# Kernel tuning notes

Hardware: AMD Instinct MI355X
Metric: run time of the kernel (lower is better)

## Reference

```python
import jax, jax.numpy as jnp
import numpy as np

D_MAX = 6.4
MASS = 40.0
GRAV = 9.8
N_PARTS = 4
B, NPTS, H, W = 512, 2048, 256, 256


def _interp(grid, xy):
    # grid: (B,H,W) over [-D_MAX,D_MAX]^2; xy: (B,N,2) -> (B,N,1) bilinear
    Bg, Hg, Wg = grid.shape
    gi = jnp.clip((xy[..., 0] + D_MAX) / (2.0 * D_MAX) * (Hg - 1), 0.0, Hg - 1.0)
    gj = jnp.clip((xy[..., 1] + D_MAX) / (2.0 * D_MAX) * (Wg - 1), 0.0, Wg - 1.0)
    i0 = jnp.clip(jnp.floor(gi).astype(jnp.int32), 0, Hg - 2)
    j0 = jnp.clip(jnp.floor(gj).astype(jnp.int32), 0, Wg - 2)
    wi = gi - i0.astype(grid.dtype)
    wj = gj - j0.astype(grid.dtype)
    flat = grid.reshape(Bg, Hg * Wg)
    gat = lambda ii, jj: jnp.take_along_axis(flat, ii * Wg + jj, axis=1)
    v = (gat(i0, j0) * (1 - wi) * (1 - wj) + gat(i0, j0 + 1) * (1 - wi) * wj
         + gat(i0 + 1, j0) * wi * (1 - wj) + gat(i0 + 1, j0 + 1) * wi * wj)
    return v[..., None]


def setup_inputs() -> dict:
    key = jax.random.key(0)
    ks = jax.random.split(key, 12)
    x = jax.random.uniform(ks[0], (B, 3), jnp.float32, -2.0, 2.0)
    xd = jax.random.normal(ks[1], (B, 3), jnp.float32)
    R, _ = jnp.linalg.qr(jax.random.normal(ks[2], (B, 3, 3), jnp.float32))
    omega = jax.random.normal(ks[3], (B, 3), jnp.float32) * 0.5
    A = jax.random.normal(ks[4], (B, 3, 3), jnp.float32) * 0.3
    I = jnp.einsum('bij,bkj->bik', A, A) + 2.0 * jnp.eye(3, dtype=jnp.float32)
    robot_points = jax.random.normal(ks[5], (B, NPTS, 3), jnp.float32) * 0.3
    z_grid = jax.random.normal(ks[6], (B, H, W), jnp.float32) * 0.1
    z_grid_grad = jax.random.normal(ks[7], (B, 2, H, W), jnp.float32) * 0.2
    stiffness = jax.random.uniform(ks[8], (B, H, W), jnp.float32, 500.0, 2000.0)
    damping = jax.random.uniform(ks[9], (B, H, W), jnp.float32, 10.0, 100.0)
    friction = jax.random.uniform(ks[10], (B, H, W), jnp.float32, 0.2, 1.0)
    driving_parts = jax.random.randint(ks[11], (NPTS,), 0, N_PARTS, jnp.int32)
    controls = jax.random.normal(jax.random.fold_in(key, 99), (B, N_PARTS), jnp.float32) * 2.0
    return dict(x=x, xd=xd, R=R, omega=omega, I=I, robot_points=robot_points,
                z_grid=z_grid, z_grid_grad=z_grid_grad, stiffness=stiffness,
                damping=damping, friction=friction, driving_parts=driving_parts,
                controls=controls)


def reference(x, xd, R, omega, I, robot_points, z_grid, z_grid_grad,
              stiffness, damping, friction, driving_parts, controls):
    n_pts = robot_points.shape[1]
    # local_to_global
    x_points = jnp.einsum('bij,bnj->bni', R, robot_points) + x[:, None]  # (B,N,3)
    xy = x_points[..., :2]
    z_points = _interp(z_grid, xy)              # (B,N,1)
    k_pts = _interp(stiffness, xy)
    d_pts = _interp(damping, xy)
    mu_pts = _interp(friction, xy)
    dh = x_points[..., 2:3] - z_points
    on_grid = ((x_points[..., 0:1] >= -D_MAX) & (x_points[..., 0:1] <= D_MAX)
               & (x_points[..., 1:2] >= -D_MAX) & (x_points[..., 1:2] <= D_MAX))
    in_contact = ((dh <= 0.0) & on_grid).astype(x.dtype)
    # surface normals from heightmap gradient: n = normalize([-dz/dx, -dz/dy, 1])
    gx = _interp(z_grid_grad[:, 0], xy)
    gy = _interp(z_grid_grad[:, 1], xy)
    n = jnp.concatenate([-gx, -gy, jnp.ones_like(gx)], axis=-1)
    n = n / jnp.linalg.norm(n, axis=-1, keepdims=True)
    # point velocities
    xd_points = xd[:, None] + jnp.cross(omega[:, None], x_points - x[:, None])
    xd_points_n = jnp.sum(xd_points * n, axis=-1, keepdims=True)
    F_spring = -(k_pts * dh + d_pts * xd_points_n) * n
    F_spring = F_spring * in_contact / n_pts
    thrust_dir = R[..., 0] / jnp.linalg.norm(R[..., 0], axis=-1, keepdims=True)
    Nmag = jnp.linalg.norm(F_spring, axis=2)  # (B,N)
    F_friction = jnp.zeros_like(F_spring)
    for i in range(N_PARTS):
        v_cmd = controls[:, i:i + 1] * thrust_dir          # (B,3)
        dv = v_cmd[:, None] - xd_points                     # (B,N,3)
        dv_n = jnp.sum(dv * n, axis=-1, keepdims=True)
        dv_tau = dv - dv_n * n
        Fi = mu_pts * Nmag[..., None] * jnp.tanh(dv_tau)
        mask = (driving_parts == i)[None, :, None]
        F_friction = jnp.where(mask, Fi, F_friction)
    torque = jnp.sum(jnp.cross(x_points - x[:, None], F_spring + F_friction), axis=1)
    I_inv = jnp.linalg.inv(I)
    omega_d = jnp.einsum('bij,bj->bi', I_inv, torque)
    F_grav = jnp.array([0.0, 0.0, -MASS * GRAV], dtype=x.dtype)
    F_cog = F_grav + F_spring.sum(axis=1) + F_friction.sum(axis=1)
    xdd = F_cog / MASS
    return (xd, xdd, omega_d, F_spring, F_friction)
```

## Files before the change

### kernel.cpp

```cpp
#include <hip/hip_runtime.h>

#pragma clang fp contract(off)

static constexpr int Bc    = 512;
static constexpr int NPTSc = 2048;
static constexpr int Hc    = 256;
static constexpr int Wc    = 256;
static constexpr float DMAXF = 6.4f;
static constexpr int CELLS = 2048;

__device__ __forceinline__ float bl(float g00, float g01, float g10, float g11,
                                    float wi, float wj) {
#pragma clang fp contract(off)
    return g00 * (1.0f - wi) * (1.0f - wj)
         + g01 * (1.0f - wi) * wj
         + g10 * wi * (1.0f - wj)
         + g11 * wi * wj;
}

__global__ __launch_bounds__(256)
void phys_points(const float* __restrict__ x, const float* __restrict__ xd,
                 const float* __restrict__ R, const float* __restrict__ omega,
                 const float* __restrict__ rp,
                 const float* __restrict__ zg, const float* __restrict__ zgg,
                 const float* __restrict__ kg, const float* __restrict__ dg,
                 const float* __restrict__ mug,
                 const int* __restrict__ dparts, const float* __restrict__ ctrl,
                 float* __restrict__ outFs, float* __restrict__ outFf,
                 float* __restrict__ partial)
{
#pragma clang fp contract(off)
    __shared__ float sg[6 * CELLS];
    __shared__ int sbox[4];

    const int tid = threadIdx.x;
    const int b = blockIdx.x >> 3;
    const int n = ((blockIdx.x & 7) << 8) + tid;

    float xb0 = x[b * 3 + 0], xb1 = x[b * 3 + 1], xb2 = x[b * 3 + 2];
    float xd0 = xd[b * 3 + 0], xd1 = xd[b * 3 + 1], xd2 = xd[b * 3 + 2];
    float om0 = omega[b * 3 + 0], om1 = omega[b * 3 + 1], om2 = omega[b * 3 + 2];
    float R00 = R[b * 9 + 0], R01 = R[b * 9 + 1], R02 = R[b * 9 + 2];
    float R10 = R[b * 9 + 3], R11 = R[b * 9 + 4], R12 = R[b * 9 + 5];
    float R20 = R[b * 9 + 6], R21 = R[b * 9 + 7], R22 = R[b * 9 + 8];

    const int part = dparts[n];
    const float cpart = ctrl[b * 4 + part];

    const int pbase = (b * NPTSc + n) * 3;
    float p0 = rp[pbase + 0], p1 = rp[pbase + 1], p2 = rp[pbase + 2];

    float xp0 = (R00 * p0 + R01 * p1 + R02 * p2) + xb0;
    float xp1 = (R10 * p0 + R11 * p1 + R12 * p2) + xb1;
    float xp2 = (R20 * p0 + R21 * p1 + R22 * p2) + xb2;

    float rx = xp0 - xb0, ry = xp1 - xb1, rz = xp2 - xb2;

    float gi = (xp0 + DMAXF) / (2.0f * DMAXF) * 255.0f;
    gi = fminf(fmaxf(gi, 0.0f), 255.0f);
    float gj = (xp1 + DMAXF) / (2.0f * DMAXF) * 255.0f;
    gj = fminf(fmaxf(gj, 0.0f), 255.0f);
    int i0 = (int)floorf(gi); i0 = min(max(i0, 0), Hc - 2);
    int j0 = (int)floorf(gj); j0 = min(max(j0, 0), Wc - 2);
    float wi = gi - (float)i0;
    float wj = gj - (float)j0;

    int mni = i0, mxi = i0, mnj = j0, mxj = j0;
    #pragma unroll
    for (int off = 32; off > 0; off >>= 1) {
        mni = min(mni, __shfl_xor(mni, off, 64));
        mxi = max(mxi, __shfl_xor(mxi, off, 64));
        mnj = min(mnj, __shfl_xor(mnj, off, 64));
        mxj = max(mxj, __shfl_xor(mxj, off, 64));
    }
    if (tid == 0) { sbox[0] = 255; sbox[1] = 0; sbox[2] = 255; sbox[3] = 0; }
    __syncthreads();
    if ((tid & 63) == 0) {
        atomicMin(&sbox[0], mni); atomicMax(&sbox[1], mxi);
        atomicMin(&sbox[2], mnj); atomicMax(&sbox[3], mxj);
    }
    __syncthreads();
    const int bmin_i = sbox[0], bmin_j = sbox[2];
    const int ih = sbox[1] - bmin_i + 2;
    const int jw = sbox[3] - bmin_j + 2;
    const bool use_lds = (ih * jw) <= CELLS;

    const int gb  = b * (Hc * Wc);
    const int gb2 = b * (2 * Hc * Wc);
    const float* planes[6] = { zg + gb, kg + gb, dg + gb, mug + gb,
                               zgg + gb2, zgg + gb2 + Hc * Wc };

    float cv[6][4];
    if (use_lds) {
        const int tx = tid & 63, ty = tid >> 6;
        #pragma unroll
        for (int p = 0; p < 6; ++p) {
            const float* src = planes[p] + bmin_i * Wc + bmin_j;
            float* dst = sg + p * CELLS;
            for (int r = ty; r < ih; r += 4)
                for (int c = tx; c < jw; c += 64)
                    dst[r * jw + c] = src[r * Wc + c];
        }
        __syncthreads();
        const int la = (i0 - bmin_i) * jw + (j0 - bmin_j);
        #pragma unroll
        for (int p = 0; p < 6; ++p) {
            const float* s = sg + p * CELLS + la;
            cv[p][0] = s[0]; cv[p][1] = s[1];
            cv[p][2] = s[jw]; cv[p][3] = s[jw + 1];
        }
    } else {
        const int la = i0 * Wc + j0;
        #pragma unroll
        for (int p = 0; p < 6; ++p) {
            const float* s = planes[p] + la;
            cv[p][0] = s[0]; cv[p][1] = s[1];
            cv[p][2] = s[Wc]; cv[p][3] = s[Wc + 1];
        }
    }

    float zp  = bl(cv[0][0], cv[0][1], cv[0][2], cv[0][3], wi, wj);
    float kp  = bl(cv[1][0], cv[1][1], cv[1][2], cv[1][3], wi, wj);
    float dpv = bl(cv[2][0], cv[2][1], cv[2][2], cv[2][3], wi, wj);
    float mup = bl(cv[3][0], cv[3][1], cv[3][2], cv[3][3], wi, wj);
    float gx  = bl(cv[4][0], cv[4][1], cv[4][2], cv[4][3], wi, wj);
    float gy  = bl(cv[5][0], cv[5][1], cv[5][2], cv[5][3], wi, wj);

    float dh = xp2 - zp;
    bool on_grid = (xp0 >= -DMAXF) && (xp0 <= DMAXF) &&
                   (xp1 >= -DMAXF) && (xp1 <= DMAXF);
    float contact = ((dh <= 0.0f) && on_grid) ? 1.0f : 0.0f;

    float nx = -gx, ny = -gy, nz = 1.0f;
    float nn = sqrtf(nx * nx + ny * ny + nz * nz);
    nx /= nn; ny /= nn; nz /= nn;

    float vx = xd0 + (om1 * rz - om2 * ry);
    float vy = xd1 + (om2 * rx - om0 * rz);
    float vz = xd2 + (om0 * ry - om1 * rx);

    float xdn = vx * nx + vy * ny + vz * nz;
    float s = -(kp * dh + dpv * xdn);
    const float scale = contact * (1.0f / 2048.0f);
    float Fs0 = (s * nx) * scale;
    float Fs1 = (s * ny) * scale;
    float Fs2 = (s * nz) * scale;

    float Nmag = sqrtf(Fs0 * Fs0 + Fs1 * Fs1 + Fs2 * Fs2);

    float t0 = R00, t1 = R10, t2 = R20;
    float tn = sqrtf(t0 * t0 + t1 * t1 + t2 * t2);
    t0 /= tn; t1 /= tn; t2 /= tn;

    float dv0 = cpart * t0 - vx;
    float dv1 = cpart * t1 - vy;
    float dv2 = cpart * t2 - vz;
    float dvn = dv0 * nx + dv1 * ny + dv2 * nz;
    float dt0 = dv0 - dvn * nx;
    float dt1 = dv1 - dvn * ny;
    float dt2 = dv2 - dvn * nz;
    float mN = mup * Nmag;
    float Ff0 = mN * tanhf(dt0);
    float Ff1 = mN * tanhf(dt1);
    float Ff2 = mN * tanhf(dt2);

    outFs[pbase + 0] = Fs0;
    outFs[pbase + 1] = Fs1;
    outFs[pbase + 2] = Fs2;
    outFf[pbase + 0] = Ff0;
    outFf[pbase + 1] = Ff1;
    outFf[pbase + 2] = Ff2;

    float Ft0 = Fs0 + Ff0, Ft1 = Fs1 + Ff1, Ft2 = Fs2 + Ff2;
    float vals[9];
    vals[0] = ry * Ft2 - rz * Ft1;
    vals[1] = rz * Ft0 - rx * Ft2;
    vals[2] = rx * Ft1 - ry * Ft0;
    vals[3] = Fs0; vals[4] = Fs1; vals[5] = Fs2;
    vals[6] = Ff0; vals[7] = Ff1; vals[8] = Ff2;

    #pragma unroll
    for (int k = 0; k < 9; ++k) {
        float v = vals[k];
        #pragma unroll
        for (int off = 32; off > 0; off >>= 1)
            v += __shfl_xor(v, off, 64);
        vals[k] = v;
    }
    if ((tid & 63) == 0) {
        const int widx = ((blockIdx.x & 7) << 2) + (tid >> 6);
        float* pb = partial + ((size_t)(b * 32 + widx)) * 9;
        #pragma unroll
        for (int k = 0; k < 9; ++k) pb[k] = vals[k];
    }
}

__global__ __launch_bounds__(64)
void phys_final(const float* __restrict__ xd, const float* __restrict__ Imat,
                const float* __restrict__ partial,
                float* __restrict__ out_xd, float* __restrict__ out_xdd,
                float* __restrict__ out_omd)
{
#pragma clang fp contract(off)
    const int b = blockIdx.x;
    const int lane = threadIdx.x;

    float v[9];
    if (lane < 32) {
        const float* pb = partial + ((size_t)(b * 32 + lane)) * 9;
        #pragma unroll
        for (int k = 0; k < 9; ++k) v[k] = pb[k];
    } else {
        #pragma unroll
        for (int k = 0; k < 9; ++k) v[k] = 0.0f;
    }
    #pragma unroll
    for (int k = 0; k < 9; ++k) {
        float t = v[k];
        #pragma unroll
        for (int off = 32; off > 0; off >>= 1)
            t += __shfl_xor(t, off, 64);
        v[k] = t;
    }

    if (lane == 0) {
        float tq0 = v[0], tq1 = v[1], tq2 = v[2];
        float sFs0 = v[3], sFs1 = v[4], sFs2 = v[5];
        float sFf0 = v[6], sFf1 = v[7], sFf2 = v[8];

        float a00 = Imat[b * 9 + 0], a01 = Imat[b * 9 + 1], a02 = Imat[b * 9 + 2];
        float a10 = Imat[b * 9 + 3], a11 = Imat[b * 9 + 4], a12 = Imat[b * 9 + 5];
        float a20 = Imat[b * 9 + 6], a21 = Imat[b * 9 + 7], a22 = Imat[b * 9 + 8];

        float c00 = a11 * a22 - a12 * a21;
        float c01 = a02 * a21 - a01 * a22;
        float c02 = a01 * a12 - a02 * a11;
        float c10 = a12 * a20 - a10 * a22;
        float c11 = a00 * a22 - a02 * a20;
        float c12 = a02 * a10 - a00 * a12;
        float c20 = a10 * a21 - a11 * a20;
        float c21 = a01 * a20 - a00 * a21;
        float c22 = a00 * a11 - a01 * a10;
        float det = a00 * c00 + a01 * c10 + a02 * c20;
        float id = 1.0f / det;

        float od0 = (c00 * tq0 + c01 * tq1 + c02 * tq2) * id;
        float od1 = (c10 * tq0 + c11 * tq1 + c12 * tq2) * id;
        float od2 = (c20 * tq0 + c21 * tq1 + c22 * tq2) * id;

        float fc0 = (0.0f + sFs0) + sFf0;
        float fc1 = (0.0f + sFs1) + sFf1;
        float fc2 = (-40.0f * 9.8f + sFs2) + sFf2;
        float xdd0 = fc0 / 40.0f, xdd1 = fc1 / 40.0f, xdd2 = fc2 / 40.0f;

        out_xd[b * 3 + 0] = xd[b * 3 + 0];
        out_xd[b * 3 + 1] = xd[b * 3 + 1];
        out_xd[b * 3 + 2] = xd[b * 3 + 2];
        out_xdd[b * 3 + 0] = xdd0;
        out_xdd[b * 3 + 1] = xdd1;
        out_xdd[b * 3 + 2] = xdd2;
        out_omd[b * 3 + 0] = od0;
        out_omd[b * 3 + 1] = od1;
        out_omd[b * 3 + 2] = od2;
    }
}

extern "C" void kernel_launch(void* const* d_in, const int* in_sizes, int n_in,
                              void* d_out, int out_size, void* d_ws, size_t ws_size,
                              hipStream_t stream)
{
    const float* x    = (const float*)d_in[0];
    const float* xd   = (const float*)d_in[1];
    const float* R    = (const float*)d_in[2];
    const float* om   = (const float*)d_in[3];
    const float* Imat = (const float*)d_in[4];
    const float* rp   = (const float*)d_in[5];
    const float* zg   = (const float*)d_in[6];
    const float* zgg  = (const float*)d_in[7];
    const float* kg   = (const float*)d_in[8];
    const float* dg   = (const float*)d_in[9];
    const float* mug  = (const float*)d_in[10];
    const int* dparts = (const int*)d_in[11];
    const float* ctrl = (const float*)d_in[12];

    float* out = (float*)d_out;
    const int B3 = Bc * 3;
    float* out_xd  = out;
    float* out_xdd = out + B3;
    float* out_omd = out + 2 * B3;
    float* outFs   = out + 3 * B3;
    float* outFf   = out + 3 * B3 + (size_t)Bc * NPTSc * 3;

    float* partial = (float*)d_ws;

    phys_points<<<Bc * NPTSc / 256, 256, 0, stream>>>(
        x, xd, R, om, rp, zg, zgg, kg, dg, mug, dparts, ctrl, outFs, outFf, partial);
    phys_final<<<Bc, 64, 0, stream>>>(
        xd, Imat, partial, out_xd, out_xdd, out_omd);
}
```

Before: 693.5 us.

## Process two points per thread with larger blocks and fixed-pitch LDS window

Blocks grow to 512 threads covering 1024 points of one batch (two points per thread), so each staged LDS grid window is shared by more points and fewer blocks repeat the staging. The LDS window becomes a fixed 48x64 tile with pitch 64, copied with a fully unrolled, row-coalesced loop. Each thread accumulates its two points before the wave reduction, which halves the partial sums written for the final kernel. The cost is more registers per thread, less parallelism, and a higher chance that a block's bounding box exceeds the tile and drops to direct global gathers.

```diff
diff --git a/kernel.cpp b/kernel.cpp
--- a/kernel.cpp
+++ b/kernel.cpp
@@ -7,7 +7,9 @@
 static constexpr int Hc    = 256;
 static constexpr int Wc    = 256;
 static constexpr float DMAXF = 6.4f;
-static constexpr int CELLS = 2048;
+static constexpr int WROWS = 48;
+static constexpr int WCOLS = 64;
+static constexpr int CELLS = WROWS * WCOLS;
 
 __device__ __forceinline__ float bl(float g00, float g01, float g10, float g11,
                                     float wi, float wj) {
@@ -18,7 +20,7 @@
          + g11 * wi * wj;
 }
 
-__global__ __launch_bounds__(256)
+__global__ __launch_bounds__(512, 4)
 void phys_points(const float* __restrict__ x, const float* __restrict__ xd,
                  const float* __restrict__ R, const float* __restrict__ omega,
                  const float* __restrict__ rp,
@@ -34,8 +36,8 @@
     __shared__ int sbox[4];
 
     const int tid = threadIdx.x;
-    const int b = blockIdx.x >> 3;
-    const int n = ((blockIdx.x & 7) << 8) + tid;
+    const int b = blockIdx.x >> 1;
+    const int nb = ((blockIdx.x & 1) << 10) + tid;
 
     float xb0 = x[b * 3 + 0], xb1 = x[b * 3 + 1], xb2 = x[b * 3 + 2];
     float xd0 = xd[b * 3 + 0], xd1 = xd[b * 3 + 1], xd2 = xd[b * 3 + 2];
@@ -44,28 +46,32 @@
     float R10 = R[b * 9 + 3], R11 = R[b * 9 + 4], R12 = R[b * 9 + 5];
     float R20 = R[b * 9 + 6], R21 = R[b * 9 + 7], R22 = R[b * 9 + 8];
 
-    const int part = dparts[n];
-    const float cpart = ctrl[b * 4 + part];
-
-    const int pbase = (b * NPTSc + n) * 3;
-    float p0 = rp[pbase + 0], p1 = rp[pbase + 1], p2 = rp[pbase + 2];
-
-    float xp0 = (R00 * p0 + R01 * p1 + R02 * p2) + xb0;
-    float xp1 = (R10 * p0 + R11 * p1 + R12 * p2) + xb1;
-    float xp2 = (R20 * p0 + R21 * p1 + R22 * p2) + xb2;
-
-    float rx = xp0 - xb0, ry = xp1 - xb1, rz = xp2 - xb2;
-
-    float gi = (xp0 + DMAXF) / (2.0f * DMAXF) * 255.0f;
-    gi = fminf(fmaxf(gi, 0.0f), 255.0f);
-    float gj = (xp1 + DMAXF) / (2.0f * DMAXF) * 255.0f;
-    gj = fminf(fmaxf(gj, 0.0f), 255.0f);
-    int i0 = (int)floorf(gi); i0 = min(max(i0, 0), Hc - 2);
-    int j0 = (int)floorf(gj); j0 = min(max(j0, 0), Wc - 2);
-    float wi = gi - (float)i0;
-    float wj = gj - (float)j0;
-
-    int mni = i0, mxi = i0, mnj = j0, mxj = j0;
+    float t0 = R00, t1 = R10, t2 = R20;
+    float tn = sqrtf(t0 * t0 + t1 * t1 + t2 * t2);
+    t0 /= tn; t1 /= tn; t2 /= tn;
+
+    float pa[2][3];
+    int i0a[2], j0a[2];
+    #pragma unroll
+    for (int k = 0; k < 2; ++k) {
+        const int n = nb + (k << 9);
+        const int pbase = (b * NPTSc + n) * 3;
+        pa[k][0] = rp[pbase + 0];
+        pa[k][1] = rp[pbase + 1];
+        pa[k][2] = rp[pbase + 2];
+        float xp0 = (R00 * pa[k][0] + R01 * pa[k][1] + R02 * pa[k][2]) + xb0;
+        float xp1 = (R10 * pa[k][0] + R11 * pa[k][1] + R12 * pa[k][2]) + xb1;
+        float gi = (xp0 + DMAXF) / (2.0f * DMAXF) * 255.0f;
+        gi = fminf(fmaxf(gi, 0.0f), 255.0f);
+        float gj = (xp1 + DMAXF) / (2.0f * DMAXF) * 255.0f;
+        gj = fminf(fmaxf(gj, 0.0f), 255.0f);
+        int i0 = (int)floorf(gi); i0 = min(max(i0, 0), Hc - 2);
+        int j0 = (int)floorf(gj); j0 = min(max(j0, 0), Wc - 2);
+        i0a[k] = i0; j0a[k] = j0;
+    }
+
+    int mni = min(i0a[0], i0a[1]), mxi = max(i0a[0], i0a[1]);
+    int mnj = min(j0a[0], j0a[1]), mxj = max(j0a[0], j0a[1]);
     #pragma unroll
     for (int off = 32; off > 0; off >>= 1) {
         mni = min(mni, __shfl_xor(mni, off, 64));
@@ -83,115 +89,148 @@
     const int bmin_i = sbox[0], bmin_j = sbox[2];
     const int ih = sbox[1] - bmin_i + 2;
     const int jw = sbox[3] - bmin_j + 2;
-    const bool use_lds = (ih * jw) <= CELLS;
+    const bool use_lds = (ih <= WROWS) && (jw <= WCOLS);
 
     const int gb  = b * (Hc * Wc);
     const int gb2 = b * (2 * Hc * Wc);
     const float* planes[6] = { zg + gb, kg + gb, dg + gb, mug + gb,
                                zgg + gb2, zgg + gb2 + Hc * Wc };
 
-    float cv[6][4];
     if (use_lds) {
-        const int tx = tid & 63, ty = tid >> 6;
+        const int c  = tid & 63;
+        const int r0 = tid >> 6;
+        const int gcol = bmin_j + c;
+        const bool cok = (gcol < Wc);
         #pragma unroll
         for (int p = 0; p < 6; ++p) {
-            const float* src = planes[p] + bmin_i * Wc + bmin_j;
-            float* dst = sg + p * CELLS;
-            for (int r = ty; r < ih; r += 4)
-                for (int c = tx; c < jw; c += 64)
-                    dst[r * jw + c] = src[r * Wc + c];
+            const float* src = planes[p] + bmin_j;
+            float* dst = sg + p * CELLS + c;
+            #pragma unroll
+            for (int pass = 0; pass < WROWS / 8; ++pass) {
+                const int r = r0 + pass * 8;
+                const int grow = bmin_i + r;
+                if (cok && grow < Hc)
+                    dst[r * WCOLS] = src[grow * Wc + c];
+            }
         }
         __syncthreads();
-        const int la = (i0 - bmin_i) * jw + (j0 - bmin_j);
-        #pragma unroll
-        for (int p = 0; p < 6; ++p) {
-            const float* s = sg + p * CELLS + la;
-            cv[p][0] = s[0]; cv[p][1] = s[1];
-            cv[p][2] = s[jw]; cv[p][3] = s[jw + 1];
+    }
+
+    float vsum[9];
+    #pragma unroll
+    for (int k = 0; k < 9; ++k) vsum[k] = 0.0f;
+
+    #pragma unroll
+    for (int k = 0; k < 2; ++k) {
+        const int n = nb + (k << 9);
+        const int pbase = (b * NPTSc + n) * 3;
+        const float p0 = pa[k][0], p1 = pa[k][1], p2 = pa[k][2];
+
+        const int part = dparts[n];
+        const float cpart = ctrl[b * 4 + part];
+
+        float xp0 = (R00 * p0 + R01 * p1 + R02 * p2) + xb0;
+        float xp1 = (R10 * p0 + R11 * p1 + R12 * p2) + xb1;
+        float xp2 = (R20 * p0 + R21 * p1 + R22 * p2) + xb2;
+
+        float rx = xp0 - xb0, ry = xp1 - xb1, rz = xp2 - xb2;
+
+        float gi = (xp0 + DMAXF) / (2.0f * DMAXF) * 255.0f;
+        gi = fminf(fmaxf(gi, 0.0f), 255.0f);
+        float gj = (xp1 + DMAXF) / (2.0f * DMAXF) * 255.0f;
+        gj = fminf(fmaxf(gj, 0.0f), 255.0f);
+        const int i0 = i0a[k], j0 = j0a[k];
+        float wi = gi - (float)i0;
+        float wj = gj - (float)j0;
+
+        float cv[6][4];
+        if (use_lds) {
+            const int la = (i0 - bmin_i) * WCOLS + (j0 - bmin_j);
+            #pragma unroll
+            for (int p = 0; p < 6; ++p) {
+                const float* s = sg + p * CELLS + la;
+                cv[p][0] = s[0];     cv[p][1] = s[1];
+                cv[p][2] = s[WCOLS]; cv[p][3] = s[WCOLS + 1];
+            }
+        } else {
+            const int la = i0 * Wc + j0;
+            #pragma unroll
+            for (int p = 0; p < 6; ++p) {
+                const float* s = planes[p] + la;
+                cv[p][0] = s[0];  cv[p][1] = s[1];
+                cv[p][2] = s[Wc]; cv[p][3] = s[Wc + 1];
+            }
         }
-    } else {
-        const int la = i0 * Wc + j0;
-        #pragma unroll
-        for (int p = 0; p < 6; ++p) {
-            const float* s = planes[p] + la;
-            cv[p][0] = s[0]; cv[p][1] = s[1];
-            cv[p][2] = s[Wc]; cv[p][3] = s[Wc + 1];
-        }
-    }
-
-    float zp  = bl(cv[0][0], cv[0][1], cv[0][2], cv[0][3], wi, wj);
-    float kp  = bl(cv[1][0], cv[1][1], cv[1][2], cv[1][3], wi, wj);
-    float dpv = bl(cv[2][0], cv[2][1], cv[2][2], cv[2][3], wi, wj);
-    float mup = bl(cv[3][0], cv[3][1], cv[3][2], cv[3][3], wi, wj);
-    float gx  = bl(cv[4][0], cv[4][1], cv[4][2], cv[4][3], wi, wj);
-    float gy  = bl(cv[5][0], cv[5][1], cv[5][2], cv[5][3], wi, wj);
-
-    float dh = xp2 - zp;
-    bool on_grid = (xp0 >= -DMAXF) && (xp0 <= DMAXF) &&
-                   (xp1 >= -DMAXF) && (xp1 <= DMAXF);
-    float contact = ((dh <= 0.0f) && on_grid) ? 1.0f : 0.0f;
-
-    float nx = -gx, ny = -gy, nz = 1.0f;
-    float nn = sqrtf(nx * nx + ny * ny + nz * nz);
-    nx /= nn; ny /= nn; nz /= nn;
-
-    float vx = xd0 + (om1 * rz - om2 * ry);
-    float vy = xd1 + (om2 * rx - om0 * rz);
-    float vz = xd2 + (om0 * ry - om1 * rx);
-
-    float xdn = vx * nx + vy * ny + vz * nz;
-    float s = -(kp * dh + dpv * xdn);
-    const float scale = contact * (1.0f / 2048.0f);
-    float Fs0 = (s * nx) * scale;
-    float Fs1 = (s * ny) * scale;
-    float Fs2 = (s * nz) * scale;
-
-    float Nmag = sqrtf(Fs0 * Fs0 + Fs1 * Fs1 + Fs2 * Fs2);
-
-    float t0 = R00, t1 = R10, t2 = R20;
-    float tn = sqrtf(t0 * t0 + t1 * t1 + t2 * t2);
-    t0 /= tn; t1 /= tn; t2 /= tn;
-
-    float dv0 = cpart * t0 - vx;
-    float dv1 = cpart * t1 - vy;
-    float dv2 = cpart * t2 - vz;
-    float dvn = dv0 * nx + dv1 * ny + dv2 * nz;
-    float dt0 = dv0 - dvn * nx;
-    float dt1 = dv1 - dvn * ny;
-    float dt2 = dv2 - dvn * nz;
-    float mN = mup * Nmag;
-    float Ff0 = mN * tanhf(dt0);
-    float Ff1 = mN * tanhf(dt1);
-    float Ff2 = mN * tanhf(dt2);
-
-    outFs[pbase + 0] = Fs0;
-    outFs[pbase + 1] = Fs1;
-    outFs[pbase + 2] = Fs2;
-    outFf[pbase + 0] = Ff0;
-    outFf[pbase + 1] = Ff1;
-    outFf[pbase + 2] = Ff2;
-
-    float Ft0 = Fs0 + Ff0, Ft1 = Fs1 + Ff1, Ft2 = Fs2 + Ff2;
-    float vals[9];
-    vals[0] = ry * Ft2 - rz * Ft1;
-    vals[1] = rz * Ft0 - rx * Ft2;
-    vals[2] = rx * Ft1 - ry * Ft0;
-    vals[3] = Fs0; vals[4] = Fs1; vals[5] = Fs2;
-    vals[6] = Ff0; vals[7] = Ff1; vals[8] = Ff2;
-
-    #pragma unroll
-    for (int k = 0; k < 9; ++k) {
-        float v = vals[k];
+
+        float zp  = bl(cv[0][0], cv[0][1], cv[0][2], cv[0][3], wi, wj);
+        float kp  = bl(cv[1][0], cv[1][1], cv[1][2], cv[1][3], wi, wj);
+        float dpv = bl(cv[2][0], cv[2][1], cv[2][2], cv[2][3], wi, wj);
+        float mup = bl(cv[3][0], cv[3][1], cv[3][2], cv[3][3], wi, wj);
+        float gx  = bl(cv[4][0], cv[4][1], cv[4][2], cv[4][3], wi, wj);
+        float gy  = bl(cv[5][0], cv[5][1], cv[5][2], cv[5][3], wi, wj);
+
+        float dh = xp2 - zp;
+        bool on_grid = (xp0 >= -DMAXF) && (xp0 <= DMAXF) &&
+                       (xp1 >= -DMAXF) && (xp1 <= DMAXF);
+        float contact = ((dh <= 0.0f) && on_grid) ? 1.0f : 0.0f;
+
+        float nx = -gx, ny = -gy, nz = 1.0f;
+        float nn = sqrtf(nx * nx + ny * ny + nz * nz);
+        nx /= nn; ny /= nn; nz /= nn;
+
+        float vx = xd0 + (om1 * rz - om2 * ry);
+        float vy = xd1 + (om2 * rx - om0 * rz);
+        float vz = xd2 + (om0 * ry - om1 * rx);
+
+        float xdn = vx * nx + vy * ny + vz * nz;
+        float s = -(kp * dh + dpv * xdn);
+        const float scale = contact * (1.0f / 2048.0f);
+        float Fs0 = (s * nx) * scale;
+        float Fs1 = (s * ny) * scale;
+        float Fs2 = (s * nz) * scale;
+
+        float Nmag = sqrtf(Fs0 * Fs0 + Fs1 * Fs1 + Fs2 * Fs2);
+
+        float dv0 = cpart * t0 - vx;
+        float dv1 = cpart * t1 - vy;
+        float dv2 = cpart * t2 - vz;
+        float dvn = dv0 * nx + dv1 * ny + dv2 * nz;
+        float dt0 = dv0 - dvn * nx;
+        float dt1 = dv1 - dvn * ny;
+        float dt2 = dv2 - dvn * nz;
+        float mN = mup * Nmag;
+        float Ff0 = mN * tanhf(dt0);
+        float Ff1 = mN * tanhf(dt1);
+        float Ff2 = mN * tanhf(dt2);
+
+        outFs[pbase + 0] = Fs0;
+        outFs[pbase + 1] = Fs1;
+        outFs[pbase + 2] = Fs2;
+        outFf[pbase + 0] = Ff0;
+        outFf[pbase + 1] = Ff1;
+        outFf[pbase + 2] = Ff2;
+
+        float Ft0 = Fs0 + Ff0, Ft1 = Fs1 + Ff1, Ft2 = Fs2 + Ff2;
+        vsum[0] += ry * Ft2 - rz * Ft1;
+        vsum[1] += rz * Ft0 - rx * Ft2;
+        vsum[2] += rx * Ft1 - ry * Ft0;
+        vsum[3] += Fs0; vsum[4] += Fs1; vsum[5] += Fs2;
+        vsum[6] += Ff0; vsum[7] += Ff1; vsum[8] += Ff2;
+    }
+
+    #pragma unroll
+    for (int kk = 0; kk < 9; ++kk) {
+        float v = vsum[kk];
         #pragma unroll
         for (int off = 32; off > 0; off >>= 1)
             v += __shfl_xor(v, off, 64);
-        vals[k] = v;
+        vsum[kk] = v;
     }
     if ((tid & 63) == 0) {
-        const int widx = ((blockIdx.x & 7) << 2) + (tid >> 6);
-        float* pb = partial + ((size_t)(b * 32 + widx)) * 9;
-        #pragma unroll
-        for (int k = 0; k < 9; ++k) pb[k] = vals[k];
+        const int widx = ((blockIdx.x & 1) << 3) + (tid >> 6);
+        float* pb = partial + ((size_t)(b * 16 + widx)) * 9;
+        #pragma unroll
+        for (int kk = 0; kk < 9; ++kk) pb[kk] = vsum[kk];
     }
 }
 
@@ -206,8 +245,8 @@
     const int lane = threadIdx.x;
 
     float v[9];
-    if (lane < 32) {
-        const float* pb = partial + ((size_t)(b * 32 + lane)) * 9;
+    if (lane < 16) {
+        const float* pb = partial + ((size_t)(b * 16 + lane)) * 9;
         #pragma unroll
         for (int k = 0; k < 9; ++k) v[k] = pb[k];
     } else {
@@ -293,7 +332,7 @@
 
     float* partial = (float*)d_ws;
 
-    phys_points<<<Bc * NPTSc / 256, 256, 0, stream>>>(
+    phys_points<<<Bc * 2, 512, 0, stream>>>(
         x, xd, R, om, rp, zg, zgg, kg, dg, mug, dparts, ctrl, outFs, outFf, partial);
     phys_final<<<Bc, 64, 0, stream>>>(
         xd, Imat, partial, out_xd, out_xdd, out_omd);
```

Measured after the change: 586.6 us. 15.4% less time.
